# Kernel optimization log

Hardware: AMD Instinct MI355X
Metric: run time of the kernel (lower is better)

Reference implementation:

```python
import jax, jax.numpy as jnp
import numpy as np

DT = 0.1
V_TH = 20.0
TAU_M = 20.0
TAU_SYN = 5.0
SYN_DECAY = float(np.exp(-DT / TAU_SYN))


@jax.custom_vjp
def surrogate_spike(v):
    # Heaviside forward
    return (v >= V_TH).astype(v.dtype)


def _ss_fwd(v):
    return surrogate_spike(v), v


def _ss_bwd(v, g):
    s = jax.nn.sigmoid(5.0 * (v - V_TH))
    return (g * s * (1.0 - s) * 5.0,)


surrogate_spike.defvjp(_ss_fwd, _ss_bwd)


def setup_inputs() -> dict:
    key = jax.random.key(0)
    k1, k2, k3, k4, k5 = jax.random.split(key, 5)
    n = 4096
    B = 64
    obs = jax.random.normal(k1, (B, 2), dtype=jnp.float32)
    W_in = jax.random.normal(k2, (n, 2), dtype=jnp.float32)
    mask = (jax.random.uniform(k3, (n, n)) < 0.1).astype(jnp.float32)
    mask = mask * (1.0 - jnp.eye(n, dtype=jnp.float32))
    W_rec = jax.random.normal(k4, (n, n), dtype=jnp.float32) * mask * 0.5 / jnp.sqrt(0.1 * n)
    W_out = jax.random.normal(k5, (1, n), dtype=jnp.float32) / jnp.sqrt(n)
    return {"obs": obs, "W_in": W_in, "W_rec": W_rec, "W_out": W_out, "n_brain_steps": 50}


def reference(obs, W_in, W_rec, W_out, n_brain_steps):
    B = obs.shape[0]
    n = W_rec.shape[0]
    # input current is constant across the 50 inner brain steps
    i_in = (obs @ W_in.T) * 5.0  # [B, n]

    def step(carry, _):
        v, i_syn, last_spikes = carry
        i_rec = last_spikes @ W_rec.T  # [B, n]
        i_syn = i_syn * SYN_DECAY + i_in + i_rec
        v = v + DT * (-v + i_syn) / TAU_M
        spikes = surrogate_spike(v)
        v = v * (1.0 - spikes)  # reset
        motor = jnp.tanh(spikes @ W_out.T)  # [B, 1]
        return (v, i_syn, jax.lax.stop_gradient(spikes)), motor

    zeros = jnp.zeros((B, n), dtype=obs.dtype)
    carry0 = (zeros, zeros, zeros)
    _, motors = jax.lax.scan(step, carry0, None, length=n_brain_steps)
    # motor_acc / n_brain_steps as in run_episode
    return motors.mean(axis=0)  # [B, 1]
```

## Files before the change

kernel.cpp:

```cpp
#include <hip/hip_runtime.h>
#include <math.h>


#define NN 4096
#define BB 64
#define STEPS 50
#define NBLK 256
#define NPB 16
#define PKROW 256
#define PKSTEP (BB * PKROW)

typedef __attribute__((ext_vector_type(4))) int i32x4;

static constexpr float WMAX_C = 0.16f;
static constexpr float QHI_C  = WMAX_C / 127.0f;
static constexpr float QLO_C  = QHI_C / 256.0f;
static constexpr float SYNDEC = (float)0.9801986733067553;


__global__ __launch_bounds__(256) void quant_kernel(const float* __restrict__ W,
                                                    signed char* __restrict__ Ph,
                                                    signed char* __restrict__ Pl,
                                                    unsigned* __restrict__ flags) {
  int idx = blockIdx.x * 256 + threadIdx.x;
  float4 w4 = reinterpret_cast<const float4*>(W)[idx];
  float w[4] = {w4.x, w4.y, w4.z, w4.w};
  signed char hi[4], lo[4];
#pragma unroll
  for (int i = 0; i < 4; i++) {
    float h = rintf(w[i] * (1.0f / QHI_C));
    h = fminf(127.0f, fmaxf(-127.0f, h));
    float r = fmaf(h, -QHI_C, w[i]);
    float l = rintf(r * (1.0f / QLO_C));
    l = fminf(127.0f, fmaxf(-127.0f, l));
    hi[i] = (signed char)(int)h;
    lo[i] = (signed char)(int)l;
  }
  reinterpret_cast<char4*>(Ph)[idx] = make_char4(hi[0], hi[1], hi[2], hi[3]);
  reinterpret_cast<char4*>(Pl)[idx] = make_char4(lo[0], lo[1], lo[2], lo[3]);
  if (blockIdx.x == 0 && threadIdx.x < NBLK) flags[threadIdx.x] = 0;
}


__device__ __forceinline__ i32x4 expand16(unsigned h) {
  i32x4 a;
#pragma unroll
  for (int q = 0; q < 4; ++q) {
    unsigned nib = (h >> (4 * q)) & 0xFu;
    a[q] = (int)((nib * 0x00204081u) & 0x01010101u);
  }
  return a;
}


__global__ __launch_bounds__(1024, 1) void brain2(
    const signed char* __restrict__ Ph,
    const signed char* __restrict__ Pl,
    const float* __restrict__ obs,
    const float* __restrict__ Win,
    unsigned* __restrict__ pk,
    unsigned* __restrict__ flags) {
  const int blk = blockIdx.x;
  const int n0  = blk * NPB;
  const int t   = threadIdx.x;
  const int lane = t & 63;
  const int w    = t >> 6;
  const int l15  = lane & 15, lhi = lane >> 4;
  const int ob   = t >> 4;
  const int on   = t & 15;

  __shared__ i32x4 red[16][4][64];

  float iin = 5.0f * (obs[ob * 2 + 0] * Win[(n0 + on) * 2 + 0] +
                      obs[ob * 2 + 1] * Win[(n0 + on) * 2 + 1]);
  float v = 0.0f, isyn = 0.0f;

  const signed char* bhp = Ph + (size_t)(n0 + l15) * NN + w * 256 + lhi * 64;
  const signed char* blp = Pl + (size_t)(n0 + l15) * NN + w * 256 + lhi * 64;
  i32x4 Bh[4], Bl[4];
#pragma unroll
  for (int kc = 0; kc < 4; ++kc) {
    Bh[kc] = *reinterpret_cast<const i32x4*>(bhp + kc * 16);
    Bl[kc] = *reinterpret_cast<const i32x4*>(blp + kc * 16);
  }

  if (on == 0)
    __hip_atomic_store(pk + ob * PKROW + blk, 0u, __ATOMIC_RELAXED,
                       __HIP_MEMORY_SCOPE_AGENT);
  asm volatile("s_waitcnt vmcnt(0)" ::: "memory");
  __syncthreads();
  if (t == 0)
    __hip_atomic_store(flags + blk, 1u, __ATOMIC_RELAXED,
                       __HIP_MEMORY_SCOPE_AGENT);

  for (int s = 0; s < STEPS; ++s) {
    if (t < NBLK) {
      while (__hip_atomic_load(flags + t, __ATOMIC_RELAXED,
                               __HIP_MEMORY_SCOPE_AGENT) < (unsigned)(s + 1))
        __builtin_amdgcn_s_sleep(1);
    }
    __syncthreads();

    unsigned sb[4][4];
    const unsigned* ps = pk + (size_t)s * PKSTEP;
#pragma unroll
    for (int mt = 0; mt < 4; ++mt) {
      const unsigned* pr = ps + (mt * 16 + l15) * PKROW + w * 16 + lhi * 4;
      unsigned long long u0 = __hip_atomic_load(
          reinterpret_cast<const unsigned long long*>(pr), __ATOMIC_RELAXED,
          __HIP_MEMORY_SCOPE_AGENT);
      unsigned long long u1 = __hip_atomic_load(
          reinterpret_cast<const unsigned long long*>(pr + 2), __ATOMIC_RELAXED,
          __HIP_MEMORY_SCOPE_AGENT);
      sb[mt][0] = (unsigned)u0;
      sb[mt][1] = (unsigned)(u0 >> 32);
      sb[mt][2] = (unsigned)u1;
      sb[mt][3] = (unsigned)(u1 >> 32);
    }

    i32x4 acch[4], accl[4];
#pragma unroll
    for (int mt = 0; mt < 4; ++mt) {
      acch[mt] = (i32x4){0, 0, 0, 0};
      accl[mt] = (i32x4){0, 0, 0, 0};
    }
#pragma unroll
    for (int mt = 0; mt < 4; ++mt)
#pragma unroll
      for (int kc = 0; kc < 4; ++kc) {
        i32x4 a = expand16(sb[mt][kc]);
        acch[mt] = __builtin_amdgcn_mfma_i32_16x16x64_i8(a, Bh[kc], acch[mt], 0, 0, 0);
        accl[mt] = __builtin_amdgcn_mfma_i32_16x16x64_i8(a, Bl[kc], accl[mt], 0, 0, 0);
      }

#pragma unroll
    for (int mt = 0; mt < 4; ++mt) {
      i32x4 vi;
#pragma unroll
      for (int r = 0; r < 4; ++r) vi[r] = (acch[mt][r] << 8) + accl[mt][r];
      red[w][mt][lane] = vi;
    }
    __syncthreads();

    {
      const int mto = ob >> 4;
      const int li  = ((ob >> 2) & 3) * 16 + on;
      const int r   = ob & 3;
      int sum = 0;
#pragma unroll
      for (int ww = 0; ww < 16; ++ww) sum += red[ww][mto][li][r];

      float rec = QLO_C * (float)sum;
      float is = isyn * SYNDEC + iin + rec;
      float vv = v + (0.1f * (is - v)) / 20.0f;
      bool sp = (vv >= 20.0f);
      v = sp ? 0.0f : vv;
      isyn = is;

      unsigned long long m = __ballot(sp);
      if ((lane & 15) == 0) {
        int j = lane >> 4;
        unsigned hw = (unsigned)((m >> (16 * j)) & 0xFFFFull);
        __hip_atomic_store(pk + (size_t)(s + 1) * PKSTEP + (w * 4 + j) * PKROW + blk,
                           hw, __ATOMIC_RELAXED, __HIP_MEMORY_SCOPE_AGENT);
      }
    }
    if (s < STEPS - 1) {
      asm volatile("s_waitcnt vmcnt(0)" ::: "memory");
      __syncthreads();
      if (t == 0)
        __hip_atomic_store(flags + blk, (unsigned)(s + 2), __ATOMIC_RELAXED,
                           __HIP_MEMORY_SCOPE_AGENT);
    }
  }
}


__global__ __launch_bounds__(256) void final_pk(const unsigned* __restrict__ pk,
                                                const float* __restrict__ Wout,
                                                float* __restrict__ out) {
  int b = blockIdx.x, t = threadIdx.x;
  int lane = t & 63, wid = t >> 6;
  float wv[16];
#pragma unroll
  for (int i = 0; i < 16; ++i) wv[i] = Wout[t * 16 + i];
  __shared__ float red4[4];
  float acc = 0.0f;
  for (int s = 1; s <= STEPS; ++s) {
    unsigned h = __hip_atomic_load(pk + (size_t)s * PKSTEP + b * PKROW + t,
                                   __ATOMIC_RELAXED, __HIP_MEMORY_SCOPE_AGENT);
    float m = 0.0f;
#pragma unroll
    for (int i = 0; i < 16; ++i)
      if ((h >> i) & 1u) m += wv[i];
#pragma unroll
    for (int off = 32; off > 0; off >>= 1) m += __shfl_down(m, off);
    if (lane == 0) red4[wid] = m;
    __syncthreads();
    if (t == 0) acc += tanhf(red4[0] + red4[1] + red4[2] + red4[3]);
    __syncthreads();
  }
  if (t == 0) out[b] = acc * (1.0f / (float)STEPS);
}


__global__ __launch_bounds__(256) void init_kernel(const float* __restrict__ obs,
                                                   const float* __restrict__ Win,
                                                   float* __restrict__ iin,
                                                   float* __restrict__ v,
                                                   float* __restrict__ isyn,
                                                   signed char* __restrict__ S8a) {
  int idx = blockIdx.x * 256 + threadIdx.x;
  int b = idx >> 12, n = idx & (NN - 1);
  float o0 = obs[b * 2 + 0], o1 = obs[b * 2 + 1];
  float w0 = Win[n * 2 + 0], w1 = Win[n * 2 + 1];
  iin[idx]  = 5.0f * (o0 * w0 + o1 * w1);
  v[idx]    = 0.0f;
  isyn[idx] = 0.0f;
  S8a[idx]  = 0;
}

__global__ __launch_bounds__(1024) void step_kernel(
    const signed char* __restrict__ S8in,
    signed char* __restrict__ S8out,
    const signed char* __restrict__ Ph,
    const signed char* __restrict__ Pl,
    const float* __restrict__ iin,
    float* __restrict__ v,
    float* __restrict__ isyn,
    const float* __restrict__ Wout,
    float* __restrict__ mpart,
    int s) {
  const int blk = blockIdx.x;
  const int n0  = blk * NPB;
  const int t   = threadIdx.x;
  const int lane = t & 63;
  const int w    = t >> 6;
  const int l15  = lane & 15, lhi = lane >> 4;

  __shared__ i32x4 red[16][4][64];

  const int kbase = w * 256 + lhi * 16;
  const signed char* ap  = S8in + (size_t)l15 * NN + kbase;
  const signed char* bhp = Ph   + (size_t)(n0 + l15) * NN + kbase;
  const signed char* blp = Pl   + (size_t)(n0 + l15) * NN + kbase;

  i32x4 acch[4], accl[4];
#pragma unroll
  for (int mt = 0; mt < 4; ++mt) {
    acch[mt] = (i32x4){0, 0, 0, 0};
    accl[mt] = (i32x4){0, 0, 0, 0};
  }
#pragma unroll
  for (int kc = 0; kc < 4; ++kc) {
    i32x4 bh = *reinterpret_cast<const i32x4*>(bhp + kc * 64);
    i32x4 bl = *reinterpret_cast<const i32x4*>(blp + kc * 64);
#pragma unroll
    for (int mt = 0; mt < 4; ++mt) {
      i32x4 a = *reinterpret_cast<const i32x4*>(ap + kc * 64 + (size_t)mt * 16 * NN);
      acch[mt] = __builtin_amdgcn_mfma_i32_16x16x64_i8(a, bh, acch[mt], 0, 0, 0);
      accl[mt] = __builtin_amdgcn_mfma_i32_16x16x64_i8(a, bl, accl[mt], 0, 0, 0);
    }
  }
#pragma unroll
  for (int mt = 0; mt < 4; ++mt) {
    i32x4 vi;
#pragma unroll
    for (int r = 0; r < 4; ++r) vi[r] = (acch[mt][r] << 8) + accl[mt][r];
    red[w][mt][lane] = vi;
  }
  __syncthreads();
  {
    const int b  = t >> 4;
    const int nl = t & 15;
    const int mt = b >> 4;
    const int li = ((b >> 2) & 3) * 16 + nl;
    const int r  = b & 3;
    int sum = 0;
#pragma unroll
    for (int ww = 0; ww < 16; ++ww) sum += red[ww][mt][li][r];

    const size_t e = (size_t)b * NN + n0 + nl;
    float rec = QLO_C * (float)sum;
    float vold = v[e];
    float is = isyn[e] * SYNDEC + iin[e] + rec;
    float vv = vold + (0.1f * (is - vold)) / 20.0f;
    bool sp = (vv >= 20.0f);
    v[e]     = sp ? 0.0f : vv;
    isyn[e]  = is;
    S8out[e] = sp ? 1 : 0;

    float mot = sp ? Wout[n0 + nl] : 0.0f;
#pragma unroll
    for (int off = 1; off < 16; off <<= 1) mot += __shfl_xor(mot, off);
    if (nl == 0) mpart[((size_t)s * BB + b) * NBLK + blk] = mot;
  }
}

__global__ __launch_bounds__(256) void final_mpart(const float* __restrict__ mpart,
                                                   float* __restrict__ out) {
  int b = blockIdx.x;
  int t = threadIdx.x;
  int lane = t & 63, wid = t >> 6;
  __shared__ float red[4];
  float acc = 0.0f;
  for (int s = 0; s < STEPS; ++s) {
    float x = mpart[((size_t)s * BB + b) * NBLK + t];
#pragma unroll
    for (int off = 32; off > 0; off >>= 1) x += __shfl_down(x, off);
    if (lane == 0) red[wid] = x;
    __syncthreads();
    if (t == 0) acc += tanhf(red[0] + red[1] + red[2] + red[3]);
    __syncthreads();
  }
  if (t == 0) out[b] = acc * (1.0f / (float)STEPS);
}


extern "C" void kernel_launch(void* const* d_in, const int* in_sizes, int n_in,
                              void* d_out, int out_size, void* d_ws, size_t ws_size,
                              hipStream_t stream) {
  const float* obs  = (const float*)d_in[0];
  const float* Win  = (const float*)d_in[1];
  const float* Wrec = (const float*)d_in[2];
  const float* Wout = (const float*)d_in[3];

  char* ws = (char*)d_ws;
  size_t off = 0;
  auto alloc = [&](size_t bytes) -> void* {
    void* p = ws + off;
    off += (bytes + 255) & ~(size_t)255;
    return p;
  };
  signed char* Ph  = (signed char*)alloc((size_t)NN * NN);
  signed char* Pl  = (signed char*)alloc((size_t)NN * NN);
  unsigned* pk     = (unsigned*)alloc((size_t)(STEPS + 1) * PKSTEP * 4);
  unsigned* flags  = (unsigned*)alloc(NBLK * 4);
  float* iin       = (float*)alloc((size_t)BB * NN * 4);
  float* v         = (float*)alloc((size_t)BB * NN * 4);
  float* isyn      = (float*)alloc((size_t)BB * NN * 4);
  signed char* S8a = (signed char*)alloc((size_t)BB * NN);
  signed char* S8b = (signed char*)alloc((size_t)BB * NN);
  float* mpart     = (float*)alloc((size_t)STEPS * BB * NBLK * 4);

  quant_kernel<<<(NN * NN) / 1024, 256, 0, stream>>>(Wrec, Ph, Pl, flags);

  void* args[] = {&Ph, &Pl, (void*)&obs, (void*)&Win, &pk, &flags};
  hipError_t cerr = hipLaunchCooperativeKernel((void*)brain2, dim3(NBLK),
                                               dim3(1024), args, 0, stream);
  if (cerr == hipSuccess) {
    final_pk<<<BB, 256, 0, stream>>>(pk, Wout, (float*)d_out);
  } else {
    init_kernel<<<(BB * NN) / 256, 256, 0, stream>>>(obs, Win, iin, v, isyn, S8a);
    for (int s = 0; s < STEPS; ++s) {
      const signed char* sin = (s & 1) ? S8b : S8a;
      signed char* sout      = (s & 1) ? S8a : S8b;
      step_kernel<<<NBLK, 1024, 0, stream>>>(sin, sout, Ph, Pl, iin, v, isyn,
                                             Wout, mpart, s);
    }
    final_mpart<<<BB, 256, 0, stream>>>(mpart, (float*)d_out);
  }
}
```

Baseline: 630.4 us.

## Replace per-step flag barrier with sentinel-tagged spike words polled directly

```diff
diff --git a/kernel.cpp b/kernel.cpp
--- a/kernel.cpp
+++ b/kernel.cpp
@@ -16,12 +16,13 @@
 static constexpr float QHI_C  = WMAX_C / 127.0f;
 static constexpr float QLO_C  = QHI_C / 256.0f;
 static constexpr float SYNDEC = (float)0.9801986733067553;
+#define HIMASK 0xFFFF0000FFFF0000ull
 
 
 __global__ __launch_bounds__(256) void quant_kernel(const float* __restrict__ W,
                                                     signed char* __restrict__ Ph,
                                                     signed char* __restrict__ Pl,
-                                                    unsigned* __restrict__ flags) {
+                                                    unsigned* __restrict__ pk) {
   int idx = blockIdx.x * 256 + threadIdx.x;
   float4 w4 = reinterpret_cast<const float4*>(W)[idx];
   float w[4] = {w4.x, w4.y, w4.z, w4.w};
@@ -38,7 +39,8 @@
   }
   reinterpret_cast<char4*>(Ph)[idx] = make_char4(hi[0], hi[1], hi[2], hi[3]);
   reinterpret_cast<char4*>(Pl)[idx] = make_char4(lo[0], lo[1], lo[2], lo[3]);
-  if (blockIdx.x == 0 && threadIdx.x < NBLK) flags[threadIdx.x] = 0;
+  if (idx < (STEPS + 1) * PKSTEP)
+    pk[idx] = (idx < PKSTEP) ? 0u : 0xAAAA0000u;
 }
 
 
@@ -50,6 +52,18 @@
     a[q] = (int)((nib * 0x00204081u) & 0x01010101u);
   }
   return a;
+}
+
+__device__ __forceinline__ unsigned long long poll8(const unsigned* p) {
+  unsigned long long u = __hip_atomic_load(
+      reinterpret_cast<const unsigned long long*>(p), __ATOMIC_RELAXED,
+      __HIP_MEMORY_SCOPE_AGENT);
+  while (u & HIMASK) {
+    __builtin_amdgcn_s_sleep(1);
+    u = __hip_atomic_load(reinterpret_cast<const unsigned long long*>(p),
+                          __ATOMIC_RELAXED, __HIP_MEMORY_SCOPE_AGENT);
+  }
+  return u;
 }
 
 
@@ -58,8 +72,7 @@
     const signed char* __restrict__ Pl,
     const float* __restrict__ obs,
     const float* __restrict__ Win,
-    unsigned* __restrict__ pk,
-    unsigned* __restrict__ flags) {
+    unsigned* __restrict__ pk) {
   const int blk = blockIdx.x;
   const int n0  = blk * NPB;
   const int t   = threadIdx.x;
@@ -84,34 +97,14 @@
     Bl[kc] = *reinterpret_cast<const i32x4*>(blp + kc * 16);
   }
 
-  if (on == 0)
-    __hip_atomic_store(pk + ob * PKROW + blk, 0u, __ATOMIC_RELAXED,
-                       __HIP_MEMORY_SCOPE_AGENT);
-  asm volatile("s_waitcnt vmcnt(0)" ::: "memory");
-  __syncthreads();
-  if (t == 0)
-    __hip_atomic_store(flags + blk, 1u, __ATOMIC_RELAXED,
-                       __HIP_MEMORY_SCOPE_AGENT);
-
   for (int s = 0; s < STEPS; ++s) {
-    if (t < NBLK) {
-      while (__hip_atomic_load(flags + t, __ATOMIC_RELAXED,
-                               __HIP_MEMORY_SCOPE_AGENT) < (unsigned)(s + 1))
-        __builtin_amdgcn_s_sleep(1);
-    }
-    __syncthreads();
-
     unsigned sb[4][4];
     const unsigned* ps = pk + (size_t)s * PKSTEP;
 #pragma unroll
     for (int mt = 0; mt < 4; ++mt) {
       const unsigned* pr = ps + (mt * 16 + l15) * PKROW + w * 16 + lhi * 4;
-      unsigned long long u0 = __hip_atomic_load(
-          reinterpret_cast<const unsigned long long*>(pr), __ATOMIC_RELAXED,
-          __HIP_MEMORY_SCOPE_AGENT);
-      unsigned long long u1 = __hip_atomic_load(
-          reinterpret_cast<const unsigned long long*>(pr + 2), __ATOMIC_RELAXED,
-          __HIP_MEMORY_SCOPE_AGENT);
+      unsigned long long u0 = poll8(pr);
+      unsigned long long u1 = poll8(pr + 2);
       sb[mt][0] = (unsigned)u0;
       sb[mt][1] = (unsigned)(u0 >> 32);
       sb[mt][2] = (unsigned)u1;
@@ -165,13 +158,7 @@
                            hw, __ATOMIC_RELAXED, __HIP_MEMORY_SCOPE_AGENT);
       }
     }
-    if (s < STEPS - 1) {
-      asm volatile("s_waitcnt vmcnt(0)" ::: "memory");
-      __syncthreads();
-      if (t == 0)
-        __hip_atomic_store(flags + blk, (unsigned)(s + 2), __ATOMIC_RELAXED,
-                           __HIP_MEMORY_SCOPE_AGENT);
-    }
+    __syncthreads();
   }
 }
 
@@ -335,7 +322,6 @@
   signed char* Ph  = (signed char*)alloc((size_t)NN * NN);
   signed char* Pl  = (signed char*)alloc((size_t)NN * NN);
   unsigned* pk     = (unsigned*)alloc((size_t)(STEPS + 1) * PKSTEP * 4);
-  unsigned* flags  = (unsigned*)alloc(NBLK * 4);
   float* iin       = (float*)alloc((size_t)BB * NN * 4);
   float* v         = (float*)alloc((size_t)BB * NN * 4);
   float* isyn      = (float*)alloc((size_t)BB * NN * 4);
@@ -343,9 +329,9 @@
   signed char* S8b = (signed char*)alloc((size_t)BB * NN);
   float* mpart     = (float*)alloc((size_t)STEPS * BB * NBLK * 4);
 
-  quant_kernel<<<(NN * NN) / 1024, 256, 0, stream>>>(Wrec, Ph, Pl, flags);
-
-  void* args[] = {&Ph, &Pl, (void*)&obs, (void*)&Win, &pk, &flags};
+  quant_kernel<<<(NN * NN) / 1024, 256, 0, stream>>>(Wrec, Ph, Pl, pk);
+
+  void* args[] = {&Ph, &Pl, (void*)&obs, (void*)&Win, &pk};
   hipError_t cerr = hipLaunchCooperativeKernel((void*)brain2, dim3(NBLK),
                                                dim3(1024), args, 0, stream);
   if (cerr == hipSuccess) {
```

Measured after the change: 574.4 us. 8.9% less time.

## Use per-step flag arrays with per-wave polling and pack spike words as 32-bit

Applied to the files above, without the earlier changes.

```diff
diff --git a/kernel.cpp b/kernel.cpp
--- a/kernel.cpp
+++ b/kernel.cpp
@@ -7,8 +7,8 @@
 #define STEPS 50
 #define NBLK 256
 #define NPB 16
-#define PKROW 256
-#define PKSTEP (BB * PKROW)
+#define PKW 8192
+#define FLG 256
 
 typedef __attribute__((ext_vector_type(4))) int i32x4;
 
@@ -21,6 +21,7 @@
 __global__ __launch_bounds__(256) void quant_kernel(const float* __restrict__ W,
                                                     signed char* __restrict__ Ph,
                                                     signed char* __restrict__ Pl,
+                                                    unsigned* __restrict__ pk,
                                                     unsigned* __restrict__ flags) {
   int idx = blockIdx.x * 256 + threadIdx.x;
   float4 w4 = reinterpret_cast<const float4*>(W)[idx];
@@ -38,7 +39,8 @@
   }
   reinterpret_cast<char4*>(Ph)[idx] = make_char4(hi[0], hi[1], hi[2], hi[3]);
   reinterpret_cast<char4*>(Pl)[idx] = make_char4(lo[0], lo[1], lo[2], lo[3]);
-  if (blockIdx.x == 0 && threadIdx.x < NBLK) flags[threadIdx.x] = 0;
+  if (idx < PKW) pk[idx] = 0u;
+  if (idx < (STEPS + 1) * FLG) flags[idx] = (idx < FLG) ? 1u : 0u;
 }
 
 
@@ -84,38 +86,31 @@
     Bl[kc] = *reinterpret_cast<const i32x4*>(blp + kc * 16);
   }
 
-  if (on == 0)
-    __hip_atomic_store(pk + ob * PKROW + blk, 0u, __ATOMIC_RELAXED,
-                       __HIP_MEMORY_SCOPE_AGENT);
-  asm volatile("s_waitcnt vmcnt(0)" ::: "memory");
-  __syncthreads();
-  if (t == 0)
-    __hip_atomic_store(flags + blk, 1u, __ATOMIC_RELAXED,
-                       __HIP_MEMORY_SCOPE_AGENT);
-
   for (int s = 0; s < STEPS; ++s) {
-    if (t < NBLK) {
-      while (__hip_atomic_load(flags + t, __ATOMIC_RELAXED,
-                               __HIP_MEMORY_SCOPE_AGENT) < (unsigned)(s + 1))
+    {
+      const unsigned* fp = flags + s * FLG + w * 16;
+      unsigned f = 1;
+      for (;;) {
+        if (lane < 16)
+          f = __hip_atomic_load(fp + lane, __ATOMIC_RELAXED,
+                                __HIP_MEMORY_SCOPE_AGENT);
+        if (__all(f != 0)) break;
         __builtin_amdgcn_s_sleep(1);
-    }
-    __syncthreads();
-
+      }
+    }
+    __builtin_amdgcn_sched_barrier(0);
+    asm volatile("" ::: "memory");
+
+    const unsigned* ps = pk + (size_t)s * PKW;
+    const int sh = (l15 & 1) * 16;
     unsigned sb[4][4];
-    const unsigned* ps = pk + (size_t)s * PKSTEP;
 #pragma unroll
     for (int mt = 0; mt < 4; ++mt) {
-      const unsigned* pr = ps + (mt * 16 + l15) * PKROW + w * 16 + lhi * 4;
-      unsigned long long u0 = __hip_atomic_load(
-          reinterpret_cast<const unsigned long long*>(pr), __ATOMIC_RELAXED,
-          __HIP_MEMORY_SCOPE_AGENT);
-      unsigned long long u1 = __hip_atomic_load(
-          reinterpret_cast<const unsigned long long*>(pr + 2), __ATOMIC_RELAXED,
-          __HIP_MEMORY_SCOPE_AGENT);
-      sb[mt][0] = (unsigned)u0;
-      sb[mt][1] = (unsigned)(u0 >> 32);
-      sb[mt][2] = (unsigned)u1;
-      sb[mt][3] = (unsigned)(u1 >> 32);
+      i32x4 wd = *reinterpret_cast<const i32x4*>(
+          ps + (mt * 8 + (l15 >> 1)) * 256 + w * 16 + lhi * 4);
+#pragma unroll
+      for (int kc = 0; kc < 4; ++kc)
+        sb[mt][kc] = ((unsigned)wd[kc] >> sh) & 0xFFFFu;
     }
 
     i32x4 acch[4], accl[4];
@@ -158,20 +153,18 @@
       isyn = is;
 
       unsigned long long m = __ballot(sp);
-      if ((lane & 15) == 0) {
-        int j = lane >> 4;
-        unsigned hw = (unsigned)((m >> (16 * j)) & 0xFFFFull);
-        __hip_atomic_store(pk + (size_t)(s + 1) * PKSTEP + (w * 4 + j) * PKROW + blk,
-                           hw, __ATOMIC_RELAXED, __HIP_MEMORY_SCOPE_AGENT);
+      if ((lane & 31) == 0) {
+        int jp = lane >> 5;
+        unsigned word = (unsigned)(m >> (32 * jp));
+        __hip_atomic_store(pk + (size_t)(s + 1) * PKW + (w * 2 + jp) * 256 + blk,
+                           word, __ATOMIC_RELAXED, __HIP_MEMORY_SCOPE_AGENT);
       }
     }
-    if (s < STEPS - 1) {
-      asm volatile("s_waitcnt vmcnt(0)" ::: "memory");
-      __syncthreads();
-      if (t == 0)
-        __hip_atomic_store(flags + blk, (unsigned)(s + 2), __ATOMIC_RELAXED,
-                           __HIP_MEMORY_SCOPE_AGENT);
-    }
+    asm volatile("s_waitcnt vmcnt(0)" ::: "memory");
+    __syncthreads();
+    if (t == 0)
+      __hip_atomic_store(flags + (s + 1) * FLG + blk, 1u, __ATOMIC_RELAXED,
+                         __HIP_MEMORY_SCOPE_AGENT);
   }
 }
 
@@ -187,8 +180,8 @@
   __shared__ float red4[4];
   float acc = 0.0f;
   for (int s = 1; s <= STEPS; ++s) {
-    unsigned h = __hip_atomic_load(pk + (size_t)s * PKSTEP + b * PKROW + t,
-                                   __ATOMIC_RELAXED, __HIP_MEMORY_SCOPE_AGENT);
+    unsigned word = pk[(size_t)s * PKW + (b >> 1) * 256 + t];
+    unsigned h = (word >> ((b & 1) * 16)) & 0xFFFFu;
     float m = 0.0f;
 #pragma unroll
     for (int i = 0; i < 16; ++i)
@@ -334,8 +327,8 @@
   };
   signed char* Ph  = (signed char*)alloc((size_t)NN * NN);
   signed char* Pl  = (signed char*)alloc((size_t)NN * NN);
-  unsigned* pk     = (unsigned*)alloc((size_t)(STEPS + 1) * PKSTEP * 4);
-  unsigned* flags  = (unsigned*)alloc(NBLK * 4);
+  unsigned* pk     = (unsigned*)alloc((size_t)(STEPS + 1) * PKW * 4);
+  unsigned* flags  = (unsigned*)alloc((size_t)(STEPS + 1) * FLG * 4);
   float* iin       = (float*)alloc((size_t)BB * NN * 4);
   float* v         = (float*)alloc((size_t)BB * NN * 4);
   float* isyn      = (float*)alloc((size_t)BB * NN * 4);
@@ -343,7 +336,7 @@
   signed char* S8b = (signed char*)alloc((size_t)BB * NN);
   float* mpart     = (float*)alloc((size_t)STEPS * BB * NBLK * 4);
 
-  quant_kernel<<<(NN * NN) / 1024, 256, 0, stream>>>(Wrec, Ph, Pl, flags);
+  quant_kernel<<<(NN * NN) / 1024, 256, 0, stream>>>(Wrec, Ph, Pl, pk, flags);
 
   void* args[] = {&Ph, &Pl, (void*)&obs, (void*)&Win, &pk, &flags};
   hipError_t cerr = hipLaunchCooperativeKernel((void*)brain2, dim3(NBLK),
```

Result: faster. 507.7 us (-19.5%).
